# Performance work log

Measured on AMD Instinct MI355X. Metric: run time of the kernel, lower is better.

Reference implementation:

```python
import jax, jax.numpy as jnp
import numpy as np

B, T, D, R = 4, 2048, 1024, 32


def setup_inputs() -> dict:
    key = jax.random.key(0)
    kx, ku = jax.random.split(key)
    x = jax.random.normal(kx, (B, T, D), dtype=jnp.float32)
    # low-rank metric factor; small init so distances are moderate
    U = jax.random.normal(ku, (D, R), dtype=jnp.float32) * 0.05
    return {"x": x, "U": U}


def reference(x, U):
    # g = U @ U.T (PSD low-rank metric).
    # dist_sq[b,t,j] = (x_t - x_j)^T g (x_t - x_j)
    #               = ||U^T x_t||^2 + ||U^T x_j||^2 - 2 (U^T x_t).(U^T x_j)
    # Algebraic expansion of the original O(B*T*T*D) broadcasted diff tensor.
    y = jnp.einsum('btd,dr->btr', x, U)                # [B,T,R]
    n = jnp.sum(y * y, axis=-1)                         # [B,T]
    cross = jnp.einsum('btr,bjr->btj', y, y)            # [B,T,T]
    dist_sq = n[:, :, None] + n[:, None, :] - 2.0 * cross
    attn = jax.nn.softmax(-dist_sq, axis=-1)            # [B,T,T]
    return jnp.einsum('btj,bjd->btd', attn, x)          # [B,T,D]
```

## Files before the change

kernel.cpp:

```cpp
#include <hip/hip_runtime.h>
#include <hip/hip_bf16.h>

#define B_ 4
#define T_ 2048
#define D_ 1024
#define R_ 32
#define XP 136

typedef __attribute__((ext_vector_type(8))) short short8;
typedef __attribute__((ext_vector_type(4))) float f32x4;
typedef __attribute__((ext_vector_type(4))) unsigned short us4;
typedef __attribute__((ext_vector_type(8))) unsigned short us8;

__device__ __forceinline__ unsigned short f2bf(float f) {
  union { float f; unsigned u; } v; v.f = f;
  unsigned r = (v.u + 0x7fffu + ((v.u >> 16) & 1u)) >> 16;
  return (unsigned short)r;
}
__device__ __forceinline__ float bf2f(unsigned short h) {
  union { unsigned u; float f; } v; v.u = (unsigned)h << 16;
  return v.f;
}
__device__ __forceinline__ unsigned pk2bf(float a, float b) {
  union { __hip_bfloat162 h; unsigned u; } v;
  v.h = __float22bfloat162_rn(make_float2(a, b));
  return v.u;
}

__global__ __launch_bounds__(256)
void geo_prep(const float* __restrict__ x, const float* __restrict__ U,
              unsigned short* __restrict__ xt, float* __restrict__ ypart) {
  __shared__ unsigned short xs[128 * XP];
  __shared__ unsigned short uts[32 * XP];
  const int bb = blockIdx.y, t0 = blockIdx.x * 128, d0 = blockIdx.z * 128;
  const int tid = threadIdx.x, w = tid >> 6, lane = tid & 63;
  const int m = lane & 15, quad = lane >> 4;

  f32x4 uv[4];
  #pragma unroll
  for (int p = 0; p < 4; p++) {
    const int i4 = p * 256 + tid;
    uv[p] = *(const f32x4*)(U + (size_t)(d0 + (i4 >> 3)) * R_ + (i4 & 7) * 4);
  }
  f32x4 xv[16];
  #pragma unroll
  for (int p = 0; p < 16; p++) {
    const int i4 = p * 256 + tid;
    xv[p] = *(const f32x4*)(x + ((size_t)bb * T_ + t0 + (i4 >> 5)) * D_ + d0 + (i4 & 31) * 4);
  }
  #pragma unroll
  for (int p = 0; p < 4; p++) {
    const int i4 = p * 256 + tid; const int du = i4 >> 3, ru4 = i4 & 7;
    #pragma unroll
    for (int k = 0; k < 4; k++) uts[(ru4 * 4 + k) * XP + du] = f2bf(uv[p][k]);
  }
  #pragma unroll
  for (int p = 0; p < 16; p++) {
    const int i4 = p * 256 + tid; const int r = i4 >> 5, c4 = i4 & 31;
    union { us4 c; unsigned u[2]; } cc;
    cc.u[0] = pk2bf(xv[p][0], xv[p][1]);
    cc.u[1] = pk2bf(xv[p][2], xv[p][3]);
    *(us4*)&xs[r * XP + ((c4 >> 1) ^ (r & 7)) * 8 + (c4 & 1) * 4] = cc.c;
  }
  __syncthreads();
  {
    const int ts = tid & 15, dsb = tid >> 4;
    us8 rowv[8];
    #pragma unroll
    for (int k = 0; k < 8; k++)
      rowv[k] = *(const us8*)&xs[(ts * 8 + k) * XP + ((dsb ^ k) * 8)];
    unsigned short* xo = xt + ((size_t)bb * D_ + d0 + dsb * 8) * T_ + t0 + ts * 8;
    #pragma unroll
    for (int dd = 0; dd < 8; dd++) {
      us8 o;
      #pragma unroll
      for (int k = 0; k < 8; k++) o[k] = rowv[k][dd];
      *(us8*)(xo + (size_t)dd * T_) = o;
    }
  }
  f32x4 acc[2][2];
  #pragma unroll
  for (int i = 0; i < 2; i++)
    #pragma unroll
    for (int j = 0; j < 2; j++) acc[i][j] = (f32x4){0.f, 0.f, 0.f, 0.f};
  #pragma unroll
  for (int ks = 0; ks < 4; ks++) {
    const int ko = ks * 32 + quad * 8;
    const int go = ((ks * 4 + quad) ^ (m & 7)) * 8;
    short8 a0 = *(const short8*)&xs[(w * 32 + m) * XP + go];
    short8 a1 = *(const short8*)&xs[(w * 32 + 16 + m) * XP + go];
    short8 b0 = *(const short8*)&uts[m * XP + ko];
    short8 b1 = *(const short8*)&uts[(16 + m) * XP + ko];
    acc[0][0] = __builtin_amdgcn_mfma_f32_16x16x32_bf16(a0, b0, acc[0][0], 0, 0, 0);
    acc[0][1] = __builtin_amdgcn_mfma_f32_16x16x32_bf16(a0, b1, acc[0][1], 0, 0, 0);
    acc[1][0] = __builtin_amdgcn_mfma_f32_16x16x32_bf16(a1, b0, acc[1][0], 0, 0, 0);
    acc[1][1] = __builtin_amdgcn_mfma_f32_16x16x32_bf16(a1, b1, acc[1][1], 0, 0, 0);
  }
  #pragma unroll
  for (int tb = 0; tb < 2; tb++)
    #pragma unroll
    for (int nb = 0; nb < 2; nb++)
      *(f32x4*)(ypart + ((size_t)(blockIdx.z * B_ + bb) * R_ + nb * 16 + m) * T_
                + t0 + w * 32 + tb * 16 + quad * 4) = acc[tb][nb];
}

__global__ __launch_bounds__(256)
void geo_reduce(const float* __restrict__ ypart, unsigned short* __restrict__ ybf,
                float* __restrict__ nsq) {
  __shared__ float ls[32][36];
  const int t0 = blockIdx.x * 32, bb = blockIdx.y;
  const int tid = threadIdx.x;
  {
    const int r = tid >> 3, t4 = (tid & 7) * 4;
    f32x4 v = {0.f, 0.f, 0.f, 0.f};
    #pragma unroll
    for (int s = 0; s < 8; s++) {
      f32x4 p = *(const f32x4*)(ypart + ((size_t)(s * B_ + bb) * R_ + r) * T_ + t0 + t4);
      #pragma unroll
      for (int k = 0; k < 4; k++) v[k] += p[k];
    }
    *(f32x4*)&ls[r][t4] = v;
  }
  __syncthreads();
  const int t = tid >> 3, r4 = (tid & 7) * 4;
  us4 pk; float part = 0.f;
  #pragma unroll
  for (int k = 0; k < 4; k++) {
    const unsigned short h = f2bf(1.69864446f * ls[r4 + k][t]);
    const float bv = bf2f(h); part += bv * bv; pk[k] = h;
  }
  *(us4*)(ybf + ((size_t)bb * T_ + t0 + t) * R_ + r4) = pk;
  part += __shfl_xor(part, 1, 64);
  part += __shfl_xor(part, 2, 64);
  part += __shfl_xor(part, 4, 64);
  if ((tid & 7) == 0) nsq[bb * T_ + t0 + t] = 0.5f * part;
}

__global__ __launch_bounds__(256, 4)
void geo_fused(const unsigned short* __restrict__ ybf,
               const float* __restrict__ nsq,
               const unsigned short* __restrict__ xt,
               float* __restrict__ out) {
  __shared__ unsigned short Bs[2][128 * 64];
  __shared__ float l_s[64];
  const int bz = blockIdx.z, id = blockIdx.x;
  const int d0 = (id & 7) * 128;
  const int t0 = (id >> 3) * 64;
  const int tid = threadIdx.x, w = tid >> 6, lane = tid & 63;
  const int m = lane & 15, quad = lane >> 4;
  const int srow = lane >> 3, sslot = lane & 7;
  const int tw = w * 16;

  const unsigned short* yb = ybf + (size_t)bz * T_ * R_;
  const float* nq = nsq + bz * T_;
  const unsigned short* Xb = xt + ((size_t)bz * D_ + d0) * T_;

#define STAGE(J0, BUF) do {                                                      \
    _Pragma("unroll")                                                            \
    for (int cc = 0; cc < 4; cc++) {                                             \
      const int rbase = w * 32 + cc * 8;                                         \
      const int row = rbase + srow;                                              \
      const int sw = (sslot ^ (row & 7)) * 8;                                    \
      __builtin_amdgcn_global_load_lds(                                          \
        (const __attribute__((address_space(1))) void*)(Xb + (size_t)row * T_ + (J0) + sw), \
        (__attribute__((address_space(3))) void*)(&Bs[BUF][rbase * 64]), 16, 0, 0); \
    } } while (0)

  short8 at = *(const short8*)(yb + (size_t)(t0 + tw + m) * R_ + quad * 8);
  const float nnt = -nq[t0 + tw + m];
  f32x4 lsum4 = {0.f, 0.f, 0.f, 0.f};

  f32x4 acc[8];
  #pragma unroll
  for (int j = 0; j < 8; j++) acc[j] = (f32x4){0.f, 0.f, 0.f, 0.f};

  STAGE(0, 0);

  for (int it = 0; it < 32; ++it) {
    const int j0 = it * 64, buf = it & 1;
    short8 aj[4]; f32x4 njv[4];
    #pragma unroll
    for (int ja = 0; ja < 4; ja++) {
      const int jr = 32 * (ja >> 1) + 8 * (m >> 2) + (ja & 1) * 4 + (m & 3);
      aj[ja] = *(const short8*)(yb + (size_t)(j0 + jr) * R_ + quad * 8);
      njv[ja] = *(const f32x4*)(nq + j0 + 32 * (ja >> 1) + (ja & 1) * 4 + 8 * quad);
    }
    union { short8 s; unsigned u[4]; } pf[2];
    #pragma unroll
    for (int ja = 0; ja < 4; ja++) {
      f32x4 cin;
      #pragma unroll
      for (int r = 0; r < 4; r++) cin[r] = nnt - njv[ja][r];
      f32x4 c = __builtin_amdgcn_mfma_f32_16x16x32_bf16(aj[ja], at, cin, 0, 0, 0);
      f32x4 p;
      #pragma unroll
      for (int r = 0; r < 4; r++) {
        p[r] = __builtin_amdgcn_exp2f(c[r]);
        lsum4[r] += p[r];
      }
      pf[ja >> 1].u[(ja & 1) * 2 + 0] = pk2bf(p[0], p[1]);
      pf[ja >> 1].u[(ja & 1) * 2 + 1] = pk2bf(p[2], p[3]);
    }
    __syncthreads();
    if (it + 1 < 32) STAGE(j0 + 64, buf ^ 1);
    #pragma unroll
    for (int kb = 0; kb < 2; kb++) {
      short8 bfr[8];
      #pragma unroll
      for (int nb = 0; nb < 8; nb++)
        bfr[nb] = *(const short8*)&Bs[buf][(nb * 16 + m) * 64 + (((kb * 4 + quad) ^ (m & 7)) * 8)];
      #pragma unroll
      for (int nb = 0; nb < 8; nb++)
        acc[nb] = __builtin_amdgcn_mfma_f32_16x16x32_bf16(pf[kb].s, bfr[nb], acc[nb], 0, 0, 0);
    }
  }
  float lsum = lsum4[0] + lsum4[1] + lsum4[2] + lsum4[3];
  lsum += __shfl_xor(lsum, 16, 64);
  lsum += __shfl_xor(lsum, 32, 64);
  if (quad == 0) l_s[tw + m] = lsum;
  __syncthreads();
  {
    f32x4 lv = *(const f32x4*)&l_s[tw + quad * 4];
    f32x4 inv;
    #pragma unroll
    for (int r = 0; r < 4; r++) inv[r] = 1.f / lv[r];
    float* ob = out + ((size_t)bz * T_ + t0 + tw + quad * 4) * D_ + d0;
    #pragma unroll
    for (int nb = 0; nb < 8; nb++)
      #pragma unroll
      for (int r = 0; r < 4; r++)
        ob[(size_t)r * D_ + nb * 16 + m] = acc[nb][r] * inv[r];
  }
#undef STAGE
}

extern "C" void kernel_launch(void* const* d_in, const int* in_sizes, int n_in,
                              void* d_out, int out_size, void* d_ws, size_t ws_size,
                              hipStream_t stream) {
  const float* x = (const float*)d_in[0];
  const float* U = (const float*)d_in[1];
  float* out = (float*)d_out;

  const size_t xt_b  = (size_t)B_ * D_ * T_ * 2;
  const size_t ybf_b = (size_t)B_ * T_ * R_ * 2;
  const size_t nsq_b = (size_t)B_ * T_ * 4;
  const size_t yp_b  = (size_t)8 * B_ * R_ * T_ * 4;

  char* wp = (char*)d_ws;
  unsigned short* xtp = (unsigned short*)wp;                 wp += xt_b;
  unsigned short* ybf = (unsigned short*)wp;                 wp += ybf_b;
  float* nsq = (float*)wp;                                   wp += nsq_b;
  float* ypart = (float*)wp;                                 wp += yp_b;
  (void)ws_size; (void)in_sizes; (void)n_in; (void)out_size;

  hipLaunchKernelGGL(geo_prep, dim3(T_ / 128, B_, D_ / 128), dim3(256), 0, stream,
                     x, U, xtp, ypart);
  hipLaunchKernelGGL(geo_reduce, dim3(T_ / 32, B_), dim3(256), 0, stream,
                     ypart, ybf, nsq);
  hipLaunchKernelGGL(geo_fused, dim3((T_ / 64) * (D_ / 128), 1, B_), dim3(256), 0, stream,
                     ybf, nsq, xtp, out);
}
```

Baseline: 158.7 us.

## Software-pipeline y/norm loads and restructure LDS staging with priority hints

Restructures the main loop into a 2x-unrolled body that prefetches the next tile's y fragments and norms into alternate registers while computing the current tile. The next LDS stage is issued at the top of each iteration with a single barrier at the end. The PV MFMA block is wrapped in s_setprio to favour matrix issue. This aims to hide global load latency and cut barrier stalls, at the cost of extra registers that may lower occupancy.

```diff
diff --git a/kernel.cpp b/kernel.cpp
--- a/kernel.cpp
+++ b/kernel.cpp
@@ -166,6 +166,50 @@
         (__attribute__((address_space(3))) void*)(&Bs[BUF][rbase * 64]), 16, 0, 0); \
     } } while (0)
 
+#define BODY(IT, AJC, NJC, AJN, NJN, BUF) do {                                   \
+    if ((IT) + 1 < 32) STAGE(((IT) + 1) * 64, (BUF) ^ 1);                        \
+    {                                                                            \
+      const int jn0 = (((IT) + 1) & 31) * 64;                                    \
+      _Pragma("unroll")                                                          \
+      for (int ja = 0; ja < 4; ja++) {                                           \
+        const int jr = 32 * (ja >> 1) + 8 * (m >> 2) + (ja & 1) * 4 + (m & 3);   \
+        AJN[ja] = *(const short8*)(yb + (size_t)(jn0 + jr) * R_ + quad * 8);     \
+        NJN[ja] = *(const f32x4*)(nq + jn0 + 32 * (ja >> 1) + (ja & 1) * 4 + 8 * quad); \
+      }                                                                          \
+    }                                                                            \
+    {                                                                            \
+      union { short8 s; unsigned u[4]; } pf[2];                                  \
+      _Pragma("unroll")                                                          \
+      for (int ja = 0; ja < 4; ja++) {                                           \
+        f32x4 cin;                                                               \
+        _Pragma("unroll")                                                        \
+        for (int r = 0; r < 4; r++) cin[r] = nnt - NJC[ja][r];                   \
+        f32x4 c = __builtin_amdgcn_mfma_f32_16x16x32_bf16(AJC[ja], at, cin, 0, 0, 0); \
+        f32x4 p;                                                                 \
+        _Pragma("unroll")                                                        \
+        for (int r = 0; r < 4; r++) {                                            \
+          p[r] = __builtin_amdgcn_exp2f(c[r]);                                   \
+          lsum4[r] += p[r];                                                      \
+        }                                                                        \
+        pf[ja >> 1].u[(ja & 1) * 2 + 0] = pk2bf(p[0], p[1]);                     \
+        pf[ja >> 1].u[(ja & 1) * 2 + 1] = pk2bf(p[2], p[3]);                     \
+      }                                                                          \
+      __builtin_amdgcn_s_setprio(1);                                             \
+      _Pragma("unroll")                                                          \
+      for (int kb = 0; kb < 2; kb++) {                                           \
+        short8 bfr[8];                                                           \
+        _Pragma("unroll")                                                        \
+        for (int nb = 0; nb < 8; nb++)                                           \
+          bfr[nb] = *(const short8*)&Bs[BUF][(nb * 16 + m) * 64 + (((kb * 4 + quad) ^ (m & 7)) * 8)]; \
+        _Pragma("unroll")                                                        \
+        for (int nb = 0; nb < 8; nb++)                                           \
+          acc[nb] = __builtin_amdgcn_mfma_f32_16x16x32_bf16(pf[kb].s, bfr[nb], acc[nb], 0, 0, 0); \
+      }                                                                          \
+      __builtin_amdgcn_s_setprio(0);                                             \
+    }                                                                            \
+    __syncthreads();                                                             \
+  } while (0)
+
   short8 at = *(const short8*)(yb + (size_t)(t0 + tw + m) * R_ + quad * 8);
   const float nnt = -nq[t0 + tw + m];
   f32x4 lsum4 = {0.f, 0.f, 0.f, 0.f};
@@ -174,46 +218,21 @@
   #pragma unroll
   for (int j = 0; j < 8; j++) acc[j] = (f32x4){0.f, 0.f, 0.f, 0.f};
 
+  short8 ajA[4], ajB[4]; f32x4 njA[4], njB[4];
   STAGE(0, 0);
-
-  for (int it = 0; it < 32; ++it) {
-    const int j0 = it * 64, buf = it & 1;
-    short8 aj[4]; f32x4 njv[4];
-    #pragma unroll
-    for (int ja = 0; ja < 4; ja++) {
-      const int jr = 32 * (ja >> 1) + 8 * (m >> 2) + (ja & 1) * 4 + (m & 3);
-      aj[ja] = *(const short8*)(yb + (size_t)(j0 + jr) * R_ + quad * 8);
-      njv[ja] = *(const f32x4*)(nq + j0 + 32 * (ja >> 1) + (ja & 1) * 4 + 8 * quad);
-    }
-    union { short8 s; unsigned u[4]; } pf[2];
-    #pragma unroll
-    for (int ja = 0; ja < 4; ja++) {
-      f32x4 cin;
-      #pragma unroll
-      for (int r = 0; r < 4; r++) cin[r] = nnt - njv[ja][r];
-      f32x4 c = __builtin_amdgcn_mfma_f32_16x16x32_bf16(aj[ja], at, cin, 0, 0, 0);
-      f32x4 p;
-      #pragma unroll
-      for (int r = 0; r < 4; r++) {
-        p[r] = __builtin_amdgcn_exp2f(c[r]);
-        lsum4[r] += p[r];
-      }
-      pf[ja >> 1].u[(ja & 1) * 2 + 0] = pk2bf(p[0], p[1]);
-      pf[ja >> 1].u[(ja & 1) * 2 + 1] = pk2bf(p[2], p[3]);
-    }
-    __syncthreads();
-    if (it + 1 < 32) STAGE(j0 + 64, buf ^ 1);
-    #pragma unroll
-    for (int kb = 0; kb < 2; kb++) {
-      short8 bfr[8];
-      #pragma unroll
-      for (int nb = 0; nb < 8; nb++)
-        bfr[nb] = *(const short8*)&Bs[buf][(nb * 16 + m) * 64 + (((kb * 4 + quad) ^ (m & 7)) * 8)];
-      #pragma unroll
-      for (int nb = 0; nb < 8; nb++)
-        acc[nb] = __builtin_amdgcn_mfma_f32_16x16x32_bf16(pf[kb].s, bfr[nb], acc[nb], 0, 0, 0);
-    }
-  }
+  #pragma unroll
+  for (int ja = 0; ja < 4; ja++) {
+    const int jr = 32 * (ja >> 1) + 8 * (m >> 2) + (ja & 1) * 4 + (m & 3);
+    ajA[ja] = *(const short8*)(yb + (size_t)jr * R_ + quad * 8);
+    njA[ja] = *(const f32x4*)(nq + 32 * (ja >> 1) + (ja & 1) * 4 + 8 * quad);
+  }
+  __syncthreads();
+
+  for (int it2 = 0; it2 < 16; it2++) {
+    BODY(2 * it2,     ajA, njA, ajB, njB, 0);
+    BODY(2 * it2 + 1, ajB, njB, ajA, njA, 1);
+  }
+
   float lsum = lsum4[0] + lsum4[1] + lsum4[2] + lsum4[3];
   lsum += __shfl_xor(lsum, 16, 64);
   lsum += __shfl_xor(lsum, 32, 64);
@@ -231,6 +250,7 @@
       for (int r = 0; r < 4; r++)
         ob[(size_t)r * D_ + nb * 16 + m] = acc[nb][r] * inv[r];
   }
+#undef BODY
 #undef STAGE
 }
 
```

Result: slower. 477.8 us (+201.2%).

## Remap waves to a 2x2 tile of t-rows and d-columns in fused kernel

Applied to the files above, without the earlier changes.

Each wave now owns 32 query rows by 64 output columns instead of 16 rows by 128 columns. That halves the LDS B-fragment reads per wave, since each fragment is reused across two row blocks. The cost is that the score MFMA and exp2 work for each row block is now computed redundantly by the two waves sharing the same rows. This trades LDS bandwidth for doubled softmax arithmetic per wave.

```diff
diff --git a/kernel.cpp b/kernel.cpp
--- a/kernel.cpp
+++ b/kernel.cpp
@@ -149,7 +149,7 @@
   const int tid = threadIdx.x, w = tid >> 6, lane = tid & 63;
   const int m = lane & 15, quad = lane >> 4;
   const int srow = lane >> 3, sslot = lane & 7;
-  const int tw = w * 16;
+  const int th = w & 1, dh = w >> 1;
 
   const unsigned short* yb = ybf + (size_t)bz * T_ * R_;
   const float* nq = nsq + bz * T_;
@@ -166,13 +166,19 @@
         (__attribute__((address_space(3))) void*)(&Bs[BUF][rbase * 64]), 16, 0, 0); \
     } } while (0)
 
-  short8 at = *(const short8*)(yb + (size_t)(t0 + tw + m) * R_ + quad * 8);
-  const float nnt = -nq[t0 + tw + m];
-  f32x4 lsum4 = {0.f, 0.f, 0.f, 0.f};
-
-  f32x4 acc[8];
-  #pragma unroll
-  for (int j = 0; j < 8; j++) acc[j] = (f32x4){0.f, 0.f, 0.f, 0.f};
+  short8 at[2]; float nnt[2]; f32x4 lsum4[2];
+  #pragma unroll
+  for (int tb = 0; tb < 2; tb++) {
+    at[tb] = *(const short8*)(yb + (size_t)(t0 + th * 32 + tb * 16 + m) * R_ + quad * 8);
+    nnt[tb] = -nq[t0 + th * 32 + tb * 16 + m];
+    lsum4[tb] = (f32x4){0.f, 0.f, 0.f, 0.f};
+  }
+
+  f32x4 acc[2][4];
+  #pragma unroll
+  for (int i = 0; i < 2; i++)
+    #pragma unroll
+    for (int j = 0; j < 4; j++) acc[i][j] = (f32x4){0.f, 0.f, 0.f, 0.f};
 
   STAGE(0, 0);
 
@@ -185,51 +191,60 @@
       aj[ja] = *(const short8*)(yb + (size_t)(j0 + jr) * R_ + quad * 8);
       njv[ja] = *(const f32x4*)(nq + j0 + 32 * (ja >> 1) + (ja & 1) * 4 + 8 * quad);
     }
-    union { short8 s; unsigned u[4]; } pf[2];
-    #pragma unroll
-    for (int ja = 0; ja < 4; ja++) {
-      f32x4 cin;
-      #pragma unroll
-      for (int r = 0; r < 4; r++) cin[r] = nnt - njv[ja][r];
-      f32x4 c = __builtin_amdgcn_mfma_f32_16x16x32_bf16(aj[ja], at, cin, 0, 0, 0);
-      f32x4 p;
-      #pragma unroll
-      for (int r = 0; r < 4; r++) {
-        p[r] = __builtin_amdgcn_exp2f(c[r]);
-        lsum4[r] += p[r];
+    union { short8 s; unsigned u[4]; } pf[2][2];
+    #pragma unroll
+    for (int tb = 0; tb < 2; tb++) {
+      #pragma unroll
+      for (int ja = 0; ja < 4; ja++) {
+        f32x4 cin;
+        #pragma unroll
+        for (int r = 0; r < 4; r++) cin[r] = nnt[tb] - njv[ja][r];
+        f32x4 c = __builtin_amdgcn_mfma_f32_16x16x32_bf16(aj[ja], at[tb], cin, 0, 0, 0);
+        f32x4 p;
+        #pragma unroll
+        for (int r = 0; r < 4; r++) {
+          p[r] = __builtin_amdgcn_exp2f(c[r]);
+          lsum4[tb][r] += p[r];
+        }
+        pf[tb][ja >> 1].u[(ja & 1) * 2 + 0] = pk2bf(p[0], p[1]);
+        pf[tb][ja >> 1].u[(ja & 1) * 2 + 1] = pk2bf(p[2], p[3]);
       }
-      pf[ja >> 1].u[(ja & 1) * 2 + 0] = pk2bf(p[0], p[1]);
-      pf[ja >> 1].u[(ja & 1) * 2 + 1] = pk2bf(p[2], p[3]);
     }
     __syncthreads();
     if (it + 1 < 32) STAGE(j0 + 64, buf ^ 1);
     #pragma unroll
     for (int kb = 0; kb < 2; kb++) {
-      short8 bfr[8];
-      #pragma unroll
-      for (int nb = 0; nb < 8; nb++)
-        bfr[nb] = *(const short8*)&Bs[buf][(nb * 16 + m) * 64 + (((kb * 4 + quad) ^ (m & 7)) * 8)];
-      #pragma unroll
-      for (int nb = 0; nb < 8; nb++)
-        acc[nb] = __builtin_amdgcn_mfma_f32_16x16x32_bf16(pf[kb].s, bfr[nb], acc[nb], 0, 0, 0);
-    }
-  }
-  float lsum = lsum4[0] + lsum4[1] + lsum4[2] + lsum4[3];
-  lsum += __shfl_xor(lsum, 16, 64);
-  lsum += __shfl_xor(lsum, 32, 64);
-  if (quad == 0) l_s[tw + m] = lsum;
+      short8 bfr[4];
+      #pragma unroll
+      for (int nb = 0; nb < 4; nb++)
+        bfr[nb] = *(const short8*)&Bs[buf][(dh * 64 + nb * 16 + m) * 64 + (((kb * 4 + quad) ^ (m & 7)) * 8)];
+      #pragma unroll
+      for (int tb = 0; tb < 2; tb++)
+        #pragma unroll
+        for (int nb = 0; nb < 4; nb++)
+          acc[tb][nb] = __builtin_amdgcn_mfma_f32_16x16x32_bf16(pf[tb][kb].s, bfr[nb], acc[tb][nb], 0, 0, 0);
+    }
+  }
+  #pragma unroll
+  for (int tb = 0; tb < 2; tb++) {
+    float lsum = lsum4[tb][0] + lsum4[tb][1] + lsum4[tb][2] + lsum4[tb][3];
+    lsum += __shfl_xor(lsum, 16, 64);
+    lsum += __shfl_xor(lsum, 32, 64);
+    if (quad == 0 && dh == 0) l_s[th * 32 + tb * 16 + m] = lsum;
+  }
   __syncthreads();
-  {
-    f32x4 lv = *(const f32x4*)&l_s[tw + quad * 4];
+  #pragma unroll
+  for (int tb = 0; tb < 2; tb++) {
+    f32x4 lv = *(const f32x4*)&l_s[th * 32 + tb * 16 + quad * 4];
     f32x4 inv;
     #pragma unroll
     for (int r = 0; r < 4; r++) inv[r] = 1.f / lv[r];
-    float* ob = out + ((size_t)bz * T_ + t0 + tw + quad * 4) * D_ + d0;
-    #pragma unroll
-    for (int nb = 0; nb < 8; nb++)
+    float* ob = out + ((size_t)bz * T_ + t0 + th * 32 + tb * 16 + quad * 4) * D_ + d0 + dh * 64;
+    #pragma unroll
+    for (int nb = 0; nb < 4; nb++)
       #pragma unroll
       for (int r = 0; r < 4; r++)
-        ob[(size_t)r * D_ + nb * 16 + m] = acc[nb][r] * inv[r];
+        ob[(size_t)r * D_ + nb * 16 + m] = acc[tb][nb][r] * inv[r];
   }
 #undef STAGE
 }
```

After: 168.9 us. +6.4%, slower.
